# Kernel optimization log

Hardware: AMD Instinct MI355X
Metric: run time of the kernel (lower is better)

## Reference

```python
import jax, jax.numpy as jnp
import numpy as np
import math

B, C, N, T = 16, 32, 500, 10
NH, DK = 8, 8
D = NH * DK  # 64
TT = 6       # tem_size after conv_temp1 (10->6)
EPS = 1e-5


def setup_inputs() -> dict:
    key = jax.random.key(0)
    ks = jax.random.split(key, 32)
    s = 0.05
    rn = lambda k, shp: jax.random.normal(k, shp, dtype=jnp.float32) * s
    return {
        "x": jax.random.normal(ks[0], (B, C, N, T), dtype=jnp.float32),
        "A": jax.random.uniform(ks[1], (N, N), dtype=jnp.float32) / N,
        "conv1_W": rn(ks[2], (32, 32)), "conv1_b": jnp.zeros((32,), jnp.float32),
        "te1_W": rn(ks[3], (64, 32)), "te1_b": jnp.zeros((64,), jnp.float32),
        "convq_W": rn(ks[4], (64, 64, 1, 3)), "convq_b": jnp.zeros((64,), jnp.float32),
        "convk_W": rn(ks[5], (64, 64, 1, 3)), "convk_b": jnp.zeros((64,), jnp.float32),
        "linv_W": rn(ks[6], (64, 64)), "linv_b": jnp.zeros((64,), jnp.float32),
        "lino_W": rn(ks[7], (64, 64)), "lino_b": jnp.zeros((64,), jnp.float32),
        "te2_W": rn(ks[8], (32, 64)), "te2_b": jnp.zeros((32,), jnp.float32),
        "mlp_W": rn(ks[9], (64, 160)), "mlp_b": jnp.zeros((64,), jnp.float32),
        "ct1_W": rn(ks[10], (6, 10)), "ct1_b": jnp.zeros((6,), jnp.float32),
        "tat_c1_W": rn(ks[11], (32,)), "tat_c2_W": rn(ks[12], (500,)),
        "tat_w": rn(ks[13], (500, 32)), "tat_b": jnp.zeros((6, 6), jnp.float32),
        "tat_v": rn(ks[14], (6, 6)),
        "bn1_g": jnp.ones((6,), jnp.float32), "bn1_b": jnp.zeros((6,), jnp.float32),
        "bn2_g": jnp.ones((32,), jnp.float32), "bn2_b": jnp.zeros((32,), jnp.float32),
    }


def _forward(x, A, conv1_W, conv1_b, te1_W, te1_b, convq_W, convq_b, convk_W, convk_b,
             linv_W, linv_b, lino_W, lino_b, te2_W, te2_b, mlp_W, mlp_b, ct1_W, ct1_b,
             tat_c1_W, tat_c2_W, tat_w, tat_b, tat_v, bn1_g, bn1_b, bn2_g, bn2_b):
    b, c, n, t = x.shape
    c1x1 = lambda z, W, bb: jnp.einsum('bchw,oc->bohw', z, W) + bb[None, :, None, None]
    residual = c1x1(x, conv1_W, conv1_b)                      # (B,32,N,T)
    h = c1x1(x, te1_W, te1_b)                                 # (B,64,N,T)
    # --- temporal-context multi-head self-attention (att bias is 0 in source due to bug) ---
    dn = ('NCHW', 'OIHW', 'NCHW')
    q = jax.lax.conv_general_dilated(h, convq_W, (1, 1), ((0, 0), (1, 1)), dimension_numbers=dn) + convq_b[None, :, None, None]
    k = jax.lax.conv_general_dilated(h, convk_W, (1, 1), ((0, 0), (1, 1)), dimension_numbers=dn) + convk_b[None, :, None, None]
    sh = lambda z: z.reshape(b, NH, DK, n, t).transpose(0, 3, 1, 4, 2)  # (B,N,h,T,dk)
    q, k = sh(q), sh(k)
    hp = h.transpose(0, 2, 3, 1)                              # (B,N,T,64)
    v = (hp @ linv_W.T + linv_b).reshape(b, n, t, NH, DK).transpose(0, 1, 3, 2, 4)
    p = jax.nn.softmax(jnp.einsum('bnhtd,bnhsd->bnhts', q, k) / math.sqrt(DK), axis=-1)
    o = jnp.einsum('bnhts,bnhsd->bnhtd', p, v).transpose(0, 1, 3, 2, 4).reshape(b, n, t, D)
    h = (o @ lino_W.T + lino_b).transpose(0, 3, 1, 2)         # (B,64,N,T)
    h = c1x1(h, te2_W, te2_b)                                 # (B,32,N,T)
    # --- multi_gcn_d: static adjacency diffusion + per-timestep attention adjacency ---
    co = h.shape[1]
    xt = h.transpose(0, 3, 2, 1)                              # (B,T,N,C)
    att = jax.nn.softmax(jnp.einsum('btnc,btmc->btnm', xt, xt) / math.sqrt(co), axis=-1)
    outs = [h]
    z = jnp.einsum('btvc,wv->btwc', xt, A); outs.append(z.transpose(0, 3, 2, 1))
    z = jnp.einsum('btvc,wv->btwc', z, A);  outs.append(z.transpose(0, 3, 2, 1))
    z = jnp.einsum('btvc,btwv->btwc', xt, att); outs.append(z.transpose(0, 3, 2, 1))
    z = jnp.einsum('btvc,btwv->btwc', z, att);  outs.append(z.transpose(0, 3, 2, 1))
    hc = c1x1(jnp.concatenate(outs, axis=1), mlp_W, mlp_b)    # (B,64,N,T)
    g = jnp.tanh(hc[:, :co]) * jax.nn.sigmoid(hc[:, co:])     # (B,32,N,10)
    # --- conv_temp1: 1x1 conv over the time axis, 10 -> 6 ---
    g = jnp.einsum('bcnt,st->bcns', g, ct1_W) + ct1_b[None, None, None, :]  # (B,32,N,6)
    # --- TATT_1 temporal attention coefficients ---
    f1 = jnp.einsum('bcnt,c->btn', g, tat_c1_W)               # (B,6,N)
    f2 = jnp.einsum('bcnt,n->bct', g, tat_c2_W)               # (B,32,6)
    logits = jax.nn.sigmoid(jnp.einsum('btn,nc,bcs->bts', f1, tat_w, f2) + tat_b)
    logits = jnp.einsum('pt,bts->bps', tat_v, logits)         # (B,6,6)
    lp = logits.transpose(0, 2, 1)
    mu = lp.mean((0, 2), keepdims=True); var = lp.var((0, 2), keepdims=True)
    lp = (lp - mu) / jnp.sqrt(var + EPS) * bn1_g[None, :, None] + bn1_b[None, :, None]
    coefs = jax.nn.softmax(lp.transpose(0, 2, 1), axis=-1)    # (B,6,6)
    Tc = coefs.transpose(0, 2, 1)
    xo = jnp.einsum('bcnl,blq->bcnq', g, Tc)                  # (B,32,N,6)
    xo = jnp.where(xo > 0, xo, 0.01 * xo) + residual[..., -xo.shape[-1]:]
    mu = xo.mean((0, 2, 3), keepdims=True); var = xo.var((0, 2, 3), keepdims=True)
    return (xo - mu) / jnp.sqrt(var + EPS) * bn2_g[None, :, None, None] + bn2_b[None, :, None, None]


def reference(x, A, conv1_W, conv1_b, te1_W, te1_b, convq_W, convq_b, convk_W, convk_b,
              linv_W, linv_b, lino_W, lino_b, te2_W, te2_b, mlp_W, mlp_b, ct1_W, ct1_b,
              tat_c1_W, tat_c2_W, tat_w, tat_b, tat_v, bn1_g, bn1_b, bn2_g, bn2_b):
    return _forward(x, A, conv1_W, conv1_b, te1_W, te1_b, convq_W, convq_b, convk_W, convk_b,
                    linv_W, linv_b, lino_W, lino_b, te2_W, te2_b, mlp_W, mlp_b, ct1_W, ct1_b,
                    tat_c1_W, tat_c2_W, tat_w, tat_b, tat_v, bn1_g, bn1_b, bn2_g, bn2_b)
```

## Files before the change

kernel.cpp:

```cpp
#include <hip/hip_runtime.h>

typedef unsigned short u16;
typedef unsigned int u32;

__device__ __forceinline__ float b2f(u16 v) { return __uint_as_float((u32)v << 16); }
__device__ __forceinline__ float lopart(u32 u) { return __uint_as_float(u << 16); }
__device__ __forceinline__ float hipart(u32 u) { return __uint_as_float(u & 0xffff0000u); }
__device__ __forceinline__ u16 f2b(float f) {
  u32 u = __float_as_uint(f);
  u32 r = u + 0x7fffu + ((u >> 16) & 1u);
  return (u16)(r >> 16);
}
__device__ __forceinline__ u32 pk2(float a, float b) {
  return (u32)f2b(a) | ((u32)f2b(b) << 16);
}
__device__ __forceinline__ u32 cvtpk(float lo, float hi) {
  u32 r;
  asm("v_cvt_pk_bf16_f32 %0, %1, %2" : "=v"(r) : "v"(lo), "v"(hi));
  return r;
}

struct Ptrs { const void* p[29]; };

typedef __attribute__((ext_vector_type(8))) short short8;
typedef __attribute__((ext_vector_type(4))) float floatx4;

__global__ void k_resolve(const void* __restrict__ g1, int* __restrict__ dtf) {
  if (threadIdx.x == 0) {
    u32 w = *(const u32*)g1;
    *dtf = ((w & 0xffffu) != 0) ? 1 : 0;
  }
}

__global__ __launch_bounds__(256) void k_cvt(Ptrs ps, const int* __restrict__ dtf,
                                             float* __restrict__ Af, float* __restrict__ Wf) {
  bool BF = *dtf != 0;
  int i = blockIdx.x * 256 + threadIdx.x;
  if (i < 250000) {
    const void* pA = ps.p[1];
    Af[i] = BF ? b2f(((const u16*)pA)[i]) : ((const float*)pA)[i];
    return;
  }
  int j = i - 250000;
  if (j >= 65322) return;
  const int SZ[27] = {1024,32,2048,64,12288,64,12288,64,4096,64,4096,64,2048,32,
                      10240,64,60,6,32,500,16000,36,36,6,6,32,32};
  int t = 0, off = 0;
#pragma unroll
  for (int k = 0; k < 27; ++k) {
    if (t == k && j >= off + SZ[k]) { off += SZ[k]; t = k + 1; }
  }
  const void* src = ps.p[2 + t];
  int l = j - off;
  Wf[j] = BF ? b2f(((const u16*)src)[l]) : ((const float*)src)[l];
}

__global__ __launch_bounds__(256) void k_cvtx(const void* __restrict__ x, const int* __restrict__ dtf,
                                              float* __restrict__ xf) {
  bool BF = *dtf != 0;
  int i = blockIdx.x * 256 + threadIdx.x;
  if (i < 2560000) xf[i] = BF ? b2f(((const u16*)x)[i]) : ((const float*)x)[i];
}

__global__ __launch_bounds__(256) void k_pk(const float* __restrict__ Af, u16* __restrict__ Abf) {
  int i = blockIdx.x * 256 + threadIdx.x;
  if (i >= 262144) return;
  int r = i >> 9, v = i & 511;
  bool in = (r < 500) && (v < 500);
  Abf[i] = f2b(in ? Af[r * 500 + v] : 0.f);
}

__global__ __launch_bounds__(256, 4) void k_a2m(const u16* __restrict__ Abf,
                                                u16* __restrict__ A2bf) {
  __shared__ u32 blsT[8192];
  int tid = threadIdx.x;
  int c0 = blockIdx.x * 32;
  for (int i = tid; i < 8192; i += 256) {
    int c = i & 31, h = i >> 5;
    int r0 = 2 * h;
    u32 lo = Abf[r0 * 512 + c0 + c];
    u32 hi = Abf[(r0 + 1) * 512 + c0 + c];
    blsT[c * 256 + (((h & 0xFC) ^ ((c & 15) << 2)) | (h & 3))] = lo | (hi << 16);
  }
  __syncthreads();
  int lane = tid & 63, wave = tid >> 6;
  int q = lane >> 4, ln = lane & 15;
  int rbase = blockIdx.y * 64 + wave * 16;
  const u32* Au = (const u32*)Abf;
  int arow = (rbase + ln) * 256;
  union F8 { u32 u[4]; short8 s; };
  floatx4 acc[2] = {{0.f,0.f,0.f,0.f},{0.f,0.f,0.f,0.f}};
  for (int c2 = 0; c2 < 16; ++c2) {
    int hb = c2 * 16 + q * 4;
    F8 af;
#pragma unroll
    for (int i2 = 0; i2 < 4; ++i2) af.u[i2] = Au[arow + hb + i2];
#pragma unroll
    for (int t2 = 0; t2 < 2; ++t2) {
      int c = t2 * 16 + ln;
      int baseT = c * 256 + (hb ^ ((c & 15) << 2));
      F8 bf;
#pragma unroll
      for (int i2 = 0; i2 < 4; ++i2) bf.u[i2] = blsT[baseT + i2];
      acc[t2] = __builtin_amdgcn_mfma_f32_16x16x32_bf16(af.s, bf.s, acc[t2], 0, 0, 0);
    }
  }
#pragma unroll
  for (int t2 = 0; t2 < 2; ++t2) {
#pragma unroll
    for (int i2 = 0; i2 < 4; ++i2) {
      int r = rbase + q * 4 + i2;
      A2bf[r * 512 + c0 + t2 * 16 + ln] = f2b(acc[t2][i2]);
    }
  }
}

__global__ __launch_bounds__(256) void k_wprep(const float* __restrict__ Wf, float* __restrict__ WT,
                                               u16* __restrict__ WBu) {
  int i = blockIdx.x * 256 + threadIdx.x;
  if (i < 1024) {
    WT[i] = Wf[(i & 31) * 32 + (i >> 5)];
  } else if (i < 7168) {
    int j2 = i - 1024;
    int o = j2 & 63, ct = j2 >> 6;
    int c = ct / 3, tap = ct - c * 3;
    float sq = 0.f, sk = 0.f;
    for (int i2 = 0; i2 < 64; ++i2) {
      float te = Wf[1056 + i2 * 32 + c];
      sq += Wf[3168 + o * 192 + i2 * 3 + tap] * te;
      sk += Wf[15520 + o * 192 + i2 * 3 + tap] * te;
    }
    ((u32*)WT)[i] = pk2(sq, sk);
  } else if (i < 7552) {
    int j2 = i - 7168;
    int f = j2 >> 6, o = j2 & 63;
    int wbase = (f & 1) ? 15520 : 3168;
    float S0 = 0.f, S1 = 0.f, S2 = 0.f;
    for (int i2 = 0; i2 < 64; ++i2) {
      float tb = Wf[3104 + i2];
      S0 += Wf[wbase + o * 192 + i2 * 3 + 0] * tb;
      S1 += Wf[wbase + o * 192 + i2 * 3 + 1] * tb;
      S2 += Wf[wbase + o * 192 + i2 * 3 + 2] * tb;
    }
    float r;
    if (f == 0)      r = Wf[15456 + o] + S0 + S1 + S2;
    else if (f == 1) r = Wf[27808 + o] + S0 + S1 + S2;
    else if (f < 4)  r = S0;
    else             r = S2;
    WT[i] = r;
  } else if (i < 9600) {
    int j2 = i - 7552;
    int c = j2 >> 6, o = j2 & 63;
    float s = 0.f;
    for (int i2 = 0; i2 < 64; ++i2)
      s += Wf[27872 + o * 64 + i2] * Wf[1056 + i2 * 32 + c];
    WT[i] = s;
  } else if (i < 9664) {
    int o = i - 9600;
    float s = Wf[31968 + o];
    for (int i2 = 0; i2 < 64; ++i2)
      s += Wf[27872 + o * 64 + i2] * Wf[3104 + i2];
    WT[i] = s;
  } else if (i < 11712) {
    int j2 = i - 9664;
    int jj = j2 >> 5, c = j2 & 31;
    float s = 0.f;
    for (int o2 = 0; o2 < 64; ++o2)
      s += Wf[36192 + c * 64 + o2] * Wf[32032 + o2 * 64 + jj];
    WT[i] = s;
  } else if (i < 11744) {
    int c = i - 11712;
    float s = Wf[38240 + c];
    for (int o2 = 0; o2 < 64; ++o2)
      s += Wf[36192 + c * 64 + o2] * Wf[36128 + o2];
    WT[i] = s;
  } else if (i < 21984) {
    int j2 = i - 11744;
    int j = j2 & 7, lanev = (j2 >> 3) & 63, ct = (j2 >> 9) & 3, kt = j2 >> 11;
    int qv = lanev >> 4, lnv = lanev & 15;
    int o = ct * 16 + lnv, k = kt * 32 + qv * 8 + j;
    WBu[j2] = f2b(Wf[38272 + o * 160 + k]);
  }
}

__global__ __launch_bounds__(256, 5) void k_front3(
    const float* __restrict__ xf, const float* __restrict__ WT,
    const float* __restrict__ c1B,
    float* __restrict__ h3x, float* __restrict__ res6)
{
  __shared__ __align__(16) float arena[4][1920];
  int tid = threadIdx.x;
  int wave = tid >> 6, lane = tid & 63;
  float* Aw = arena[wave];
  int pair = blockIdx.x * 4 + wave;
  int b = pair / 500, n = pair - b * 500;

  const float* c1T  = WT;
  const u32*   qkF  = (const u32*)(WT + 1024);
  const float* bCq  = WT + 7168;
  const float* bCk  = WT + 7232;
  const float* bE0q = WT + 7296;
  const float* bE0k = WT + 7360;
  const float* bE2q = WT + 7424;
  const float* bE2k = WT + 7488;
  const float* vT   = WT + 7552;
  const float* bvp  = WT + 9600;
  const float* otT  = WT + 9664;
  const float* botp = WT + 11712;

  {
    int c0 = lane >> 1, hf = (lane & 1) * 5;
    const float* xp = xf + ((b * 32 + c0) * 500 + n) * 10 + hf;
    float* dst = Aw + c0 * 12 + hf;
#pragma unroll
    for (int k2 = 0; k2 < 5; ++k2) dst[k2] = xp[k2];
  }
  __builtin_amdgcn_wave_barrier();

  int cl = lane & 31, th = lane >> 5;

  {
    float r0 = c1B[cl], r1 = r0, r2 = r0;
#pragma unroll 4
    for (int i = 0; i < 32; ++i) {
      float w = c1T[i * 32 + cl];
      const float* xr = Aw + i * 12 + 4 + th * 3;
      r0 += w * xr[0]; r1 += w * xr[1]; r2 += w * xr[2];
    }
    float* rp = res6 + ((b * 32 + cl) * 500 + n) * 6 + th * 3;
    rp[0] = r0; rp[1] = r1; rp[2] = r2;
  }

  float qr[10], kr[10], vr[10];
  {
    float cq = bCq[lane], ck = bCk[lane], bv = bvp[lane];
#pragma unroll
    for (int t = 0; t < 10; ++t) { qr[t] = cq; kr[t] = ck; vr[t] = bv; }
    qr[0] -= bE0q[lane]; kr[0] -= bE0k[lane];
    qr[9] -= bE2q[lane]; kr[9] -= bE2k[lane];
    const u32* qp0 = qkF + lane;
    const float* vp0 = vT + lane;
#pragma unroll 2
    for (int c = 0; c < 32; ++c) {
      const float* xr = Aw + c * 12;
      float4 ha = *(const float4*)xr;
      float4 hb = *(const float4*)(xr + 4);
      float2 hc = *(const float2*)(xr + 8);
      u32 u0 = qp0[c * 192];
      u32 u1 = qp0[c * 192 + 64];
      u32 u2 = qp0[c * 192 + 128];
      float wv = vp0[c * 64];
      float q0 = lopart(u0), q1 = lopart(u1), q2 = lopart(u2);
      float k0 = hipart(u0), k1 = hipart(u1), k2v = hipart(u2);
      float hh[10] = {ha.x, ha.y, ha.z, ha.w, hb.x, hb.y, hb.z, hb.w, hc.x, hc.y};
#pragma unroll
      for (int t = 0; t < 10; ++t) { float c_ = hh[t]; qr[t] += q1 * c_; kr[t] += k1 * c_; vr[t] += wv * c_; }
#pragma unroll
      for (int t = 1; t < 10; ++t) { float c_ = hh[t - 1]; qr[t] += q0 * c_; kr[t] += k0 * c_; }
#pragma unroll
      for (int t = 0; t < 9; ++t) { float c_ = hh[t + 1]; qr[t] += q2 * c_; kr[t] += k2v * c_; }
    }
  }
  __builtin_amdgcn_wave_barrier();
  {
    u32* qu = (u32*)Aw + lane * 5;
#pragma unroll
    for (int m = 0; m < 5; ++m) qu[m] = pk2(qr[2 * m], qr[2 * m + 1]);
    float* kp = Aw + 320 + lane * 12;
    *(float4*)kp       = make_float4(kr[0], kr[1], kr[2], kr[3]);
    *(float4*)(kp + 4) = make_float4(kr[4], kr[5], kr[6], kr[7]);
    *(float2*)(kp + 8) = make_float2(kr[8], kr[9]);
  }
  __builtin_amdgcn_wave_barrier();

  {
    const u32* qb = (const u32*)Aw;
#pragma unroll
    for (int pass = 0; pass < 2; ++pass) {
      int row = pass * 64 + lane;
      if (row < 80) {
        int h8 = (row / 10) * 8, r = row - (row / 10) * 10;
        int rm = r >> 1, rs = r & 1;
        float sv[10];
#pragma unroll
        for (int s = 0; s < 10; ++s) sv[s] = 0.f;
#pragma unroll 2
        for (int d = 0; d < 8; ++d) {
          int jj = h8 + d;
          u32 qu = qb[jj * 5 + rm];
          float qv = rs ? hipart(qu) : lopart(qu);
          const float* kp2 = Aw + 320 + jj * 12;
          float4 ka = *(const float4*)kp2;
          float4 kb = *(const float4*)(kp2 + 4);
          float2 kc = *(const float2*)(kp2 + 8);
          sv[0] += qv * ka.x; sv[1] += qv * ka.y; sv[2] += qv * ka.z; sv[3] += qv * ka.w;
          sv[4] += qv * kb.x; sv[5] += qv * kb.y; sv[6] += qv * kb.z; sv[7] += qv * kb.w;
          sv[8] += qv * kc.x; sv[9] += qv * kc.y;
        }
        const float sc_ = 0.35355339059327373f;
        float mx = sv[0];
#pragma unroll
        for (int s = 1; s < 10; ++s) mx = fmaxf(mx, sv[s]);
        float tot = 0.f, ev[10];
#pragma unroll
        for (int s = 0; s < 10; ++s) { ev[s] = expf((sv[s] - mx) * sc_); tot += ev[s]; }
        float inv = 1.f / tot;
        float* pp = Aw + 1088 + row * 10;
#pragma unroll
        for (int s = 0; s < 10; ++s) pp[s] = ev[s] * inv;
      }
    }
  }
  __builtin_amdgcn_wave_barrier();

  {
    const float* pb = Aw + 1088 + (lane >> 3) * 100;
    float orr[10];
#pragma unroll
    for (int t = 0; t < 10; ++t) {
      const float* pr = pb + t * 10;
      float a = 0.f;
#pragma unroll
      for (int s = 0; s < 10; ++s) a += pr[s] * vr[s];
      orr[t] = a;
    }
    float* op = Aw + lane * 12;
    *(float4*)op       = make_float4(orr[0], orr[1], orr[2], orr[3]);
    *(float4*)(op + 4) = make_float4(orr[4], orr[5], orr[6], orr[7]);
    *(float2*)(op + 8) = make_float2(orr[8], orr[9]);
  }
  __builtin_amdgcn_wave_barrier();

  {
    float bt2 = botp[cl];
    float a5[5];
#pragma unroll
    for (int k2 = 0; k2 < 5; ++k2) a5[k2] = bt2;
    const float* tp0 = otT + cl;
    const float* base = Aw + th * 5;
#pragma unroll 2
    for (int j = 0; j < 64; ++j) {
      float w = tp0[j * 32];
      const float* lp = base + j * 12;
#pragma unroll
      for (int k2 = 0; k2 < 5; ++k2) a5[k2] += w * lp[k2];
    }
    int t0 = th * 5;
#pragma unroll
    for (int k2 = 0; k2 < 5; ++k2)
      h3x[((b * 10 + t0 + k2) * 500 + n) * 32 + cl] = a5[k2];
  }
}

__global__ __launch_bounds__(256, 4) void k_z12m(const float* __restrict__ h3x,
    const u16* __restrict__ Abf, const u16* __restrict__ A2bf,
    float* __restrict__ z1x, float* __restrict__ z2x) {
  __shared__ u32 xlsT[8192];
  int tid = threadIdx.x, bt = blockIdx.x;
  const float* src = h3x + bt * 16000;
  for (int i = tid; i < 8192; i += 256) {
    int n = i & 31, h = i >> 5;
    int r0 = 2 * h;
    float v0 = (r0 < 500) ? src[r0 * 32 + n] : 0.f;
    float v1 = (r0 + 1 < 500) ? src[(r0 + 1) * 32 + n] : 0.f;
    xlsT[n * 256 + (((h & 0xFC) ^ ((n & 15) << 2)) | (h & 3))] = pk2(v0, v1);
  }
  __syncthreads();
  int lane = tid & 63, wave = tid >> 6;
  int q = lane >> 4, ln = lane & 15;
  int rbase = blockIdx.y * 64 + wave * 16;
  const u32* Au = (const u32*)Abf;
  const u32* A2u = (const u32*)A2bf;
  int arow = (rbase + ln) * 256;
  union F8 { u32 u[4]; short8 s; };
  floatx4 acc1[2] = {{0.f,0.f,0.f,0.f},{0.f,0.f,0.f,0.f}};
  floatx4 acc2[2] = {{0.f,0.f,0.f,0.f},{0.f,0.f,0.f,0.f}};
  for (int c2 = 0; c2 < 16; ++c2) {
    int hb = c2 * 16 + q * 4;
    F8 a1f, a2f;
#pragma unroll
    for (int i2 = 0; i2 < 4; ++i2) {
      a1f.u[i2] = Au[arow + hb + i2];
      a2f.u[i2] = A2u[arow + hb + i2];
    }
#pragma unroll
    for (int t2 = 0; t2 < 2; ++t2) {
      int n = t2 * 16 + ln;
      int baseT = n * 256 + (hb ^ ((n & 15) << 2));
      F8 bf;
#pragma unroll
      for (int i2 = 0; i2 < 4; ++i2) bf.u[i2] = xlsT[baseT + i2];
      acc1[t2] = __builtin_amdgcn_mfma_f32_16x16x32_bf16(a1f.s, bf.s, acc1[t2], 0, 0, 0);
      acc2[t2] = __builtin_amdgcn_mfma_f32_16x16x32_bf16(a2f.s, bf.s, acc2[t2], 0, 0, 0);
    }
  }
  int outb = bt * 16000;
#pragma unroll
  for (int t2 = 0; t2 < 2; ++t2) {
#pragma unroll
    for (int i2 = 0; i2 < 4; ++i2) {
      int r = rbase + q * 4 + i2;
      if (r < 500) {
        z1x[outb + r * 32 + t2 * 16 + ln] = acc1[t2][i2];
        z2x[outb + r * 32 + t2 * 16 + ln] = acc2[t2][i2];
      }
    }
  }
}

__global__ __launch_bounds__(256, 2) void k_attn2(const float* __restrict__ keys,
                                                  const float* __restrict__ vals,
                                                  float* __restrict__ outp) {
  __shared__ u32 xls[8192];
  __shared__ u32 pch[4][272];
  int tid = threadIdx.x, bt = blockIdx.x;
  const float* kb = keys + bt * 16000;
  for (int i = tid; i < 8192; i += 256) {
    int r = i >> 4, cu = i & 15;
    u32 u = 0;
    if (r < 500) {
      float2 g = *(const float2*)(kb + r * 32 + cu * 2);
      u = pk2(g.x, g.y);
    }
    xls[(r << 4) | (cu ^ (r & 15))] = u;
  }
  __syncthreads();
  int lane = tid & 63, wave = tid >> 6;
  int q = lane >> 4, ln = lane & 15;
  int rbase = blockIdx.y * 64 + wave * 16;
  union F8 { u32 u[4]; short8 s; };
  F8 af;
  {
    int r = rbase + ln;
#pragma unroll
    for (int i2 = 0; i2 < 4; ++i2)
      af.u[i2] = xls[(r << 4) | ((q * 4 + i2) ^ (r & 15))];
  }
  floatx4 acc[32];
#pragma unroll
  for (int ct = 0; ct < 32; ++ct) {
    int r2 = ct * 16 + ln;
    F8 bf;
#pragma unroll
    for (int i2 = 0; i2 < 4; ++i2)
      bf.u[i2] = xls[(r2 << 4) | ((q * 4 + i2) ^ (r2 & 15))];
    acc[ct] = __builtin_amdgcn_mfma_f32_16x16x32_bf16(af.s, bf.s,
              (floatx4){0.f, 0.f, 0.f, 0.f}, 0, 0, 0);
  }
  if (ln >= 4) {
#pragma unroll
    for (int i2 = 0; i2 < 4; ++i2) acc[31][i2] = -1e30f;
  }
  const float sc = 0.17677669529663687f;
  float inv[4];
#pragma unroll
  for (int i2 = 0; i2 < 4; ++i2) {
    float m = -1e30f;
#pragma unroll
    for (int ct = 0; ct < 32; ++ct) m = fmaxf(m, acc[ct][i2]);
#pragma unroll
    for (int d = 1; d < 16; d <<= 1) m = fmaxf(m, __shfl_xor(m, d));
    float s = 0.f;
#pragma unroll
    for (int ct = 0; ct < 32; ++ct) {
      float e = expf((acc[ct][i2] - m) * sc);
      acc[ct][i2] = e; s += e;
    }
#pragma unroll
    for (int d = 1; d < 16; d <<= 1) s += __shfl_xor(s, d);
    inv[i2] = 1.f / s;
  }
  const float* vb = vals + bt * 16000;
  floatx4 zacc[2] = {{0.f,0.f,0.f,0.f},{0.f,0.f,0.f,0.f}};
  u32* myp = pch[wave];
  u16* pw = (u16*)myp;
  for (int c2 = 0; c2 < 16; ++c2) {
#pragma unroll
    for (int t2 = 0; t2 < 2; ++t2) {
      int ct = c2 * 2 + t2;
#pragma unroll
      for (int i2 = 0; i2 < 4; ++i2)
        pw[(q * 4 + i2) * 34 + t2 * 16 + ln] = f2b(acc[ct][i2] * inv[i2]);
    }
    __syncthreads();
    F8 pa;
#pragma unroll
    for (int i2 = 0; i2 < 4; ++i2) pa.u[i2] = myp[ln * 17 + q * 4 + i2];
    int k0 = c2 * 32 + q * 8;
#pragma unroll
    for (int t2 = 0; t2 < 2; ++t2) {
      int n = t2 * 16 + ln;
      short8 bs;
#pragma unroll
      for (int j = 0; j < 8; ++j) {
        float v = vb[(k0 + j) * 32 + n];
        bs[j] = (short)(__float_as_uint(v) >> 16);
      }
      zacc[t2] = __builtin_amdgcn_mfma_f32_16x16x32_bf16(pa.s, bs, zacc[t2], 0, 0, 0);
    }
    __syncthreads();
  }
  int outb = bt * 16000;
#pragma unroll
  for (int t2 = 0; t2 < 2; ++t2) {
#pragma unroll
    for (int i2 = 0; i2 < 4; ++i2) {
      int r = rbase + q * 4 + i2;
      if (r < 500) outp[outb + r * 32 + t2 * 16 + ln] = zacc[t2][i2];
    }
  }
}

__global__ __launch_bounds__(256, 2) void k_gate(
    const float* __restrict__ h3x, const float* __restrict__ z1x, const float* __restrict__ z2x,
    const float* __restrict__ z3x, const float* __restrict__ z4x,
    const u32* __restrict__ WBq, const float* __restrict__ mlpB,
    const float* __restrict__ ct1W, const float* __restrict__ ct1B,
    float* __restrict__ g2w)
{
  __shared__ u32 wlds[5120];
  int tid = threadIdx.x;
  for (int i = tid; i < 5120; i += 256) wlds[i] = WBq[i];
  __syncthreads();
  int lane = tid & 63, wave = tid >> 6;
  int q = lane >> 4, ln = lane & 15;
  int b = blockIdx.y;
  int n0 = blockIdx.x * 32 + wave * 8;
  int nA = n0 + (ln & 7);
  int tAb = ln >> 3;
  int nD = n0 + (q & 1) * 4;
  int tDb = q >> 1;
  float g2a[4][2][6];
#pragma unroll
  for (int i = 0; i < 4; ++i)
#pragma unroll
    for (int ch = 0; ch < 2; ++ch)
#pragma unroll
      for (int s = 0; s < 6; ++s) g2a[i][ch][s] = 0.f;
  float bias[4];
#pragma unroll
  for (int ct = 0; ct < 4; ++ct) bias[ct] = mlpB[ct * 16 + ln];
  union F8 { u32 u[4]; short8 s; };
  for (int tile = 0; tile < 5; ++tile) {
    int tA = tile * 2 + tAb;
    int offA = (((b * 10 + tA) * 500) + nA) * 32 + q * 8;
    floatx4 acc[4];
#pragma unroll
    for (int ct = 0; ct < 4; ++ct) acc[ct] = (floatx4){bias[ct], bias[ct], bias[ct], bias[ct]};
#pragma unroll
    for (int kt = 0; kt < 5; ++kt) {
      const float* sp = kt == 0 ? h3x : kt == 1 ? z1x : kt == 2 ? z2x : kt == 3 ? z3x : z4x;
      float4 a0 = *(const float4*)(sp + offA);
      float4 a1 = *(const float4*)(sp + offA + 4);
      F8 af;
      af.u[0] = cvtpk(a0.x, a0.y);
      af.u[1] = cvtpk(a0.z, a0.w);
      af.u[2] = cvtpk(a1.x, a1.y);
      af.u[3] = cvtpk(a1.z, a1.w);
#pragma unroll
      for (int ct = 0; ct < 4; ++ct) {
        F8 bfr;
        const u32* wp = wlds + (((kt * 4 + ct) << 6) + lane) * 4;
#pragma unroll
        for (int i2 = 0; i2 < 4; ++i2) bfr.u[i2] = wp[i2];
        acc[ct] = __builtin_amdgcn_mfma_f32_16x16x32_bf16(af.s, bfr.s, acc[ct], 0, 0, 0);
      }
    }
    int tD = tile * 2 + tDb;
    float c6[6];
#pragma unroll
    for (int s = 0; s < 6; ++s) c6[s] = ct1W[s * 10 + tD];
#pragma unroll
    for (int i = 0; i < 4; ++i) {
      float e0 = __expf(2.f * acc[0][i]);
      float g0 = ((e0 - 1.f) / (e0 + 1.f)) * (1.f / (1.f + __expf(-acc[2][i])));
      float e1 = __expf(2.f * acc[1][i]);
      float g1 = ((e1 - 1.f) / (e1 + 1.f)) * (1.f / (1.f + __expf(-acc[3][i])));
#pragma unroll
      for (int s = 0; s < 6; ++s) {
        g2a[i][0][s] += g0 * c6[s];
        g2a[i][1][s] += g1 * c6[s];
      }
    }
  }
#pragma unroll
  for (int i = 0; i < 4; ++i)
#pragma unroll
    for (int ch = 0; ch < 2; ++ch)
#pragma unroll
      for (int s = 0; s < 6; ++s)
        g2a[i][ch][s] += __shfl_xor(g2a[i][ch][s], 32);
  if (q < 2) {
#pragma unroll
    for (int i = 0; i < 4; ++i) {
      int n = nD + i;
      if (n < 500) {
#pragma unroll
        for (int ch = 0; ch < 2; ++ch) {
          int c = ln + ch * 16;
          float* gp = g2w + ((b * 32 + c) * 500 + n) * 6;
#pragma unroll
          for (int s = 0; s < 6; ++s) gp[s] = g2a[i][ch][s] + ct1B[s];
        }
      }
    }
  }
}

__global__ __launch_bounds__(256) void k_f1n(const float* __restrict__ g2w,
                                             const float* __restrict__ tc1W,
                                             float* __restrict__ f1w) {
  int i = blockIdx.x * 256 + threadIdx.x;
  if (i >= 48000) return;
  int b = i / 3000, rem = i - b * 3000, s = rem / 500, n = rem - s * 500;
  float a = 0.f;
  for (int c = 0; c < 32; ++c) a += g2w[((b * 32 + c) * 500 + n) * 6 + s] * tc1W[c];
  f1w[(b * 6 + s) * 500 + n] = a;
}

__global__ __launch_bounds__(64) void k_f2(const float* __restrict__ g2w,
                                           const float* __restrict__ c2W, float* __restrict__ f2w) {
  int b = blockIdx.x >> 5, c = blockIdx.x & 31, lane = threadIdx.x;
  float acc[6];
#pragma unroll
  for (int t = 0; t < 6; ++t) acc[t] = 0.f;
  for (int n = lane; n < 500; n += 64) {
    float w = c2W[n];
    const float* gp = g2w + ((b * 32 + c) * 500 + n) * 6;
#pragma unroll
    for (int t = 0; t < 6; ++t) acc[t] += w * gp[t];
  }
#pragma unroll
  for (int t = 0; t < 6; ++t)
    for (int off = 32; off; off >>= 1) acc[t] += __shfl_xor(acc[t], off);
  if (lane == 0) {
#pragma unroll
    for (int t = 0; t < 6; ++t) f2w[(b * 32 + c) * 6 + t] = acc[t];
  }
}

__global__ __launch_bounds__(256) void k_tatt(
    const float* __restrict__ f1w, const float* __restrict__ tatw,
    const float* __restrict__ f2w, const float* __restrict__ tatb, const float* __restrict__ tatv,
    float* __restrict__ lg2w)
{
  __shared__ float mid[192];
  __shared__ float lgt[36];
  int b = blockIdx.x, tid = threadIdx.x;
  if (tid < 192) {
    int t = tid >> 5, c = tid & 31;
    float a = 0.f;
    const float* f1p = f1w + (b * 6 + t) * 500;
    for (int n = 0; n < 500; ++n) a += f1p[n] * tatw[n * 32 + c];
    mid[t * 32 + c] = a;
  }
  __syncthreads();
  if (tid < 36) {
    int t = tid / 6, s = tid - t * 6;
    float a = tatb[t * 6 + s];
    for (int c = 0; c < 32; ++c) a += mid[t * 32 + c] * f2w[(b * 32 + c) * 6 + s];
    lgt[t * 6 + s] = 1.f / (1.f + expf(-a));
  }
  __syncthreads();
  if (tid < 36) {
    int p = tid / 6, s = tid - p * 6;
    float a = 0.f;
#pragma unroll
    for (int t2 = 0; t2 < 6; ++t2) a += tatv[p * 6 + t2] * lgt[t2 * 6 + s];
    lg2w[(b * 6 + p) * 6 + s] = a;
  }
}

__global__ __launch_bounds__(128) void k_coefs(const float* __restrict__ lg2w,
    const float* __restrict__ bn1g, const float* __restrict__ bn1b, float* __restrict__ tcw) {
  __shared__ float mu[6], iv[6], gg[6], bb[6];
  int tid = threadIdx.x;
  if (tid < 6) {
    float s = 0.f, sq = 0.f;
    for (int b = 0; b < 16; ++b)
      for (int q = 0; q < 6; ++q) {
        float v = lg2w[(b * 6 + q) * 6 + tid];
        s += v; sq += v * v;
      }
    float m = s / 96.f;
    mu[tid] = m;
    iv[tid] = rsqrtf(sq / 96.f - m * m + 1e-5f);
    gg[tid] = bn1g[tid]; bb[tid] = bn1b[tid];
  }
  __syncthreads();
  for (int idx = tid; idx < 96; idx += 128) {
    int b = idx / 6, q = idx - b * 6;
    float v[6], mx = -1e30f;
#pragma unroll
    for (int l = 0; l < 6; ++l) {
      v[l] = (lg2w[(b * 6 + q) * 6 + l] - mu[l]) * iv[l] * gg[l] + bb[l];
      mx = fmaxf(mx, v[l]);
    }
    float tot = 0.f;
#pragma unroll
    for (int l = 0; l < 6; ++l) { v[l] = expf(v[l] - mx); tot += v[l]; }
    float inv = 1.f / tot;
#pragma unroll
    for (int l = 0; l < 6; ++l) tcw[(b * 6 + l) * 6 + q] = v[l] * inv;
  }
}

__global__ __launch_bounds__(256) void k_xo(const float* __restrict__ g2w,
    const float* __restrict__ res6, const float* __restrict__ tcw,
    float* __restrict__ xow, float* __restrict__ stats) {
  __shared__ float Tcl[36];
  __shared__ float redS[32][8], redQ[32][8];
  int b = blockIdx.x, chunk = blockIdx.y, tid = threadIdx.x;
  if (tid < 36) Tcl[tid] = tcw[b * 36 + tid];
  __syncthreads();
  int c = tid & 31, sub = tid >> 5;
  int n0 = chunk * 50;
  float s = 0.f, sq = 0.f;
  for (int idx = sub; idx < 300; idx += 8) {
    int nl = idx / 6, q = idx - nl * 6;
    int n = n0 + nl;
    int base = ((b * 32 + c) * 500 + n) * 6;
    const float* gp = g2w + base;
    float xv = 0.f;
#pragma unroll
    for (int l = 0; l < 6; ++l) xv += gp[l] * Tcl[l * 6 + q];
    xv = xv > 0.f ? xv : 0.01f * xv;
    xv += res6[base + q];
    xow[base + q] = xv;
    s += xv; sq += xv * xv;
  }
  redS[c][sub] = s; redQ[c][sub] = sq;
  __syncthreads();
  if (sub == 0) {
    float ts = 0.f, tq = 0.f;
#pragma unroll
    for (int k = 0; k < 8; ++k) { ts += redS[c][k]; tq += redQ[c][k]; }
    atomicAdd(&stats[c], ts);
    atomicAdd(&stats[32 + c], tq);
  }
}

__global__ __launch_bounds__(256) void k_out(const float* __restrict__ xow,
    const float* __restrict__ stats, const float* __restrict__ g2c, const float* __restrict__ b2c,
    float* __restrict__ out) {
  int base = (blockIdx.x * 256 + threadIdx.x) * 4;
#pragma unroll
  for (int k = 0; k < 4; ++k) {
    int i = base + k;
    int c = (i / 3000) & 31;
    float m = stats[c] * (1.f / 48000.f);
    float var = stats[32 + c] * (1.f / 48000.f) - m * m;
    out[i] = (xow[i] - m) * rsqrtf(var + 1e-5f) * g2c[c] + b2c[c];
  }
}

extern "C" void kernel_launch(void* const* d_in, const int* in_sizes, int n_in,
                              void* d_out, int out_size, void* d_ws, size_t ws_size,
                              hipStream_t stream)
{
  (void)in_sizes; (void)out_size;

  float* ws = (float*)d_ws;
  float* Af   = ws;
  float* Wf   = Af + 250000;
  float* A2   = Wf + 65536;
  float* h3x  = A2 + 250000;
  float* z1x  = h3x + 2560000;
  float* z2x  = z1x + 2560000;
  float* z3x  = z2x + 2560000;
  float* z4x  = z3x + 2560000;
  float* res6 = z4x + 2560000;
  float* g2w  = res6 + 1536000;
  float* f1w  = g2w + 1536000;
  float* f2w  = f1w + 48000;
  float* lg2w = f2w + 3072;
  float* tcw  = lg2w + 576;
  float* stats= tcw + 576;
  int*   dtf  = (int*)(stats + 64);
  float* xf   = z4x;
  float* xow  = z1x;
  u16*   Abf  = (u16*)g2w;
  u16*   A2bf = (u16*)(g2w + 131072);
  float* WTp  = g2w + 262144;
  u16*   WBu  = (u16*)f1w;
  if (ws_size < (size_t)16489952 * sizeof(float)) return;

  const float* c1B  = Wf + 1024;
  const float* mlpB = Wf + 48512;
  const float* ct1W = Wf + 48576;
  const float* ct1B = Wf + 48636;
  const float* tc1W = Wf + 48642;
  const float* tc2W = Wf + 48674;
  const float* tatw = Wf + 49174;
  const float* tatb = Wf + 65174;
  const float* tatv = Wf + 65210;
  const float* bn1g = Wf + 65246;
  const float* bn1b = Wf + 65252;
  const float* bn2g = Wf + 65258;
  const float* bn2b = Wf + 65290;

  Ptrs ps;
  for (int i = 0; i < 29; ++i) ps.p[i] = (i < n_in) ? d_in[i] : d_in[0];

  hipMemsetAsync(stats, 0, 64 * sizeof(float), stream);
  k_resolve<<<dim3(1),     64, 0, stream>>>(ps.p[25], dtf);
  k_cvt  <<<dim3(1232),    256, 0, stream>>>(ps, dtf, Af, Wf);
  k_cvtx <<<dim3(10000),   256, 0, stream>>>(ps.p[0], dtf, xf);
  k_wprep<<<dim3(86),      256, 0, stream>>>(Wf, WTp, WBu);
  k_pk   <<<dim3(1024),    256, 0, stream>>>(Af, Abf);
  k_a2m  <<<dim3(16, 8),   256, 0, stream>>>(Abf, A2bf);
  k_front3<<<dim3(2000),   256, 0, stream>>>(xf, WTp, c1B, h3x, res6);
  k_z12m <<<dim3(160, 8),  256, 0, stream>>>(h3x, Abf, A2bf, z1x, z2x);
  k_attn2<<<dim3(160, 8),  256, 0, stream>>>(h3x, h3x, z3x);
  k_attn2<<<dim3(160, 8),  256, 0, stream>>>(h3x, z3x, z4x);
  k_gate <<<dim3(16, 16),  256, 0, stream>>>(h3x, z1x, z2x, z3x, z4x,
                                             (const u32*)WBu, mlpB, ct1W, ct1B, g2w);
  k_f1n  <<<dim3(188),     256, 0, stream>>>(g2w, tc1W, f1w);
  k_f2   <<<dim3(512),      64, 0, stream>>>(g2w, tc2W, f2w);
  k_tatt <<<dim3(16),      256, 0, stream>>>(f1w, tatw, f2w, tatb, tatv, lg2w);
  k_coefs<<<dim3(1),       128, 0, stream>>>(lg2w, bn1g, bn1b, tcw);
  k_xo   <<<dim3(16, 10),  256, 0, stream>>>(g2w, res6, tcw, xow, stats);
  k_out  <<<dim3(1500),    256, 0, stream>>>(xow, stats, bn2g, bn2b, (float*)d_out);
}
```

Baseline: 444.0 us.

## Fuse input conversion into consumers and stage V transposed in LDS for attention

Removes the separate fp32 conversion passes for x and A: k_front3 and k_pk now read raw bf16/f32 inputs directly. In k_attn2, V is loaded once per block into a transposed, swizzled bf16 LDS buffer, replacing strided global gathers in the PV loop. The block-wide syncs there become wave barriers because the P scratch is per-wave. This cuts global traffic and launches at the cost of more LDS per block, which may reduce occupancy.

```diff
diff --git a/kernel.cpp b/kernel.cpp
--- a/kernel.cpp
+++ b/kernel.cpp
@@ -33,15 +33,9 @@
 }
 
 __global__ __launch_bounds__(256) void k_cvt(Ptrs ps, const int* __restrict__ dtf,
-                                             float* __restrict__ Af, float* __restrict__ Wf) {
+                                             float* __restrict__ Wf) {
   bool BF = *dtf != 0;
-  int i = blockIdx.x * 256 + threadIdx.x;
-  if (i < 250000) {
-    const void* pA = ps.p[1];
-    Af[i] = BF ? b2f(((const u16*)pA)[i]) : ((const float*)pA)[i];
-    return;
-  }
-  int j = i - 250000;
+  int j = blockIdx.x * 256 + threadIdx.x;
   if (j >= 65322) return;
   const int SZ[27] = {1024,32,2048,64,12288,64,12288,64,4096,64,4096,64,2048,32,
                       10240,64,60,6,32,500,16000,36,36,6,6,32,32};
@@ -55,19 +49,16 @@
   Wf[j] = BF ? b2f(((const u16*)src)[l]) : ((const float*)src)[l];
 }
 
-__global__ __launch_bounds__(256) void k_cvtx(const void* __restrict__ x, const int* __restrict__ dtf,
-                                              float* __restrict__ xf) {
+__global__ __launch_bounds__(256) void k_pk(const void* __restrict__ A, const int* __restrict__ dtf,
+                                            u16* __restrict__ Abf) {
   bool BF = *dtf != 0;
-  int i = blockIdx.x * 256 + threadIdx.x;
-  if (i < 2560000) xf[i] = BF ? b2f(((const u16*)x)[i]) : ((const float*)x)[i];
-}
-
-__global__ __launch_bounds__(256) void k_pk(const float* __restrict__ Af, u16* __restrict__ Abf) {
   int i = blockIdx.x * 256 + threadIdx.x;
   if (i >= 262144) return;
   int r = i >> 9, v = i & 511;
   bool in = (r < 500) && (v < 500);
-  Abf[i] = f2b(in ? Af[r * 500 + v] : 0.f);
+  u16 o = 0;
+  if (in) o = BF ? ((const u16*)A)[r * 500 + v] : f2b(((const float*)A)[r * 500 + v]);
+  Abf[i] = o;
 }
 
 __global__ __launch_bounds__(256, 4) void k_a2m(const u16* __restrict__ Abf,
@@ -184,7 +175,7 @@
 }
 
 __global__ __launch_bounds__(256, 5) void k_front3(
-    const float* __restrict__ xf, const float* __restrict__ WT,
+    const void* __restrict__ xraw, const int* __restrict__ dtf, const float* __restrict__ WT,
     const float* __restrict__ c1B,
     float* __restrict__ h3x, float* __restrict__ res6)
 {
@@ -209,11 +200,19 @@
   const float* botp = WT + 11712;
 
   {
+    bool BF = *dtf != 0;
     int c0 = lane >> 1, hf = (lane & 1) * 5;
-    const float* xp = xf + ((b * 32 + c0) * 500 + n) * 10 + hf;
+    int base = ((b * 32 + c0) * 500 + n) * 10 + hf;
     float* dst = Aw + c0 * 12 + hf;
-#pragma unroll
-    for (int k2 = 0; k2 < 5; ++k2) dst[k2] = xp[k2];
+    if (BF) {
+      const u16* xp = (const u16*)xraw + base;
+#pragma unroll
+      for (int k2 = 0; k2 < 5; ++k2) dst[k2] = b2f(xp[k2]);
+    } else {
+      const float* xp = (const float*)xraw + base;
+#pragma unroll
+      for (int k2 = 0; k2 < 5; ++k2) dst[k2] = xp[k2];
+    }
   }
   __builtin_amdgcn_wave_barrier();
 
@@ -412,9 +411,11 @@
                                                   const float* __restrict__ vals,
                                                   float* __restrict__ outp) {
   __shared__ u32 xls[8192];
+  __shared__ u32 vlsT[8192];
   __shared__ u32 pch[4][272];
   int tid = threadIdx.x, bt = blockIdx.x;
   const float* kb = keys + bt * 16000;
+  const float* vb = vals + bt * 16000;
   for (int i = tid; i < 8192; i += 256) {
     int r = i >> 4, cu = i & 15;
     u32 u = 0;
@@ -423,6 +424,11 @@
       u = pk2(g.x, g.y);
     }
     xls[(r << 4) | (cu ^ (r & 15))] = u;
+    int n = i & 31, h = i >> 5;
+    int r0 = 2 * h;
+    float v0 = (r0 < 500) ? vb[r0 * 32 + n] : 0.f;
+    float v1 = (r0 + 1 < 500) ? vb[(r0 + 1) * 32 + n] : 0.f;
+    vlsT[n * 256 + (((h & 0xFC) ^ ((n & 15) << 2)) | (h & 3))] = pk2(v0, v1);
   }
   __syncthreads();
   int lane = tid & 63, wave = tid >> 6;
@@ -470,7 +476,6 @@
     for (int d = 1; d < 16; d <<= 1) s += __shfl_xor(s, d);
     inv[i2] = 1.f / s;
   }
-  const float* vb = vals + bt * 16000;
   floatx4 zacc[2] = {{0.f,0.f,0.f,0.f},{0.f,0.f,0.f,0.f}};
   u32* myp = pch[wave];
   u16* pw = (u16*)myp;
@@ -482,23 +487,21 @@
       for (int i2 = 0; i2 < 4; ++i2)
         pw[(q * 4 + i2) * 34 + t2 * 16 + ln] = f2b(acc[ct][i2] * inv[i2]);
     }
-    __syncthreads();
+    __builtin_amdgcn_wave_barrier();
     F8 pa;
 #pragma unroll
     for (int i2 = 0; i2 < 4; ++i2) pa.u[i2] = myp[ln * 17 + q * 4 + i2];
-    int k0 = c2 * 32 + q * 8;
+    int hb = c2 * 16 + q * 4;
 #pragma unroll
     for (int t2 = 0; t2 < 2; ++t2) {
       int n = t2 * 16 + ln;
-      short8 bs;
-#pragma unroll
-      for (int j = 0; j < 8; ++j) {
-        float v = vb[(k0 + j) * 32 + n];
-        bs[j] = (short)(__float_as_uint(v) >> 16);
-      }
-      zacc[t2] = __builtin_amdgcn_mfma_f32_16x16x32_bf16(pa.s, bs, zacc[t2], 0, 0, 0);
-    }
-    __syncthreads();
+      int baseT = n * 256 + (hb ^ ((n & 15) << 2));
+      F8 bf;
+#pragma unroll
+      for (int i2 = 0; i2 < 4; ++i2) bf.u[i2] = vlsT[baseT + i2];
+      zacc[t2] = __builtin_amdgcn_mfma_f32_16x16x32_bf16(pa.s, bf.s, zacc[t2], 0, 0, 0);
+    }
+    __builtin_amdgcn_wave_barrier();
   }
   int outb = bt * 16000;
 #pragma unroll
@@ -777,7 +780,6 @@
   float* tcw  = lg2w + 576;
   float* stats= tcw + 576;
   int*   dtf  = (int*)(stats + 64);
-  float* xf   = z4x;
   float* xow  = z1x;
   u16*   Abf  = (u16*)g2w;
   u16*   A2bf = (u16*)(g2w + 131072);
@@ -804,12 +806,11 @@
 
   hipMemsetAsync(stats, 0, 64 * sizeof(float), stream);
   k_resolve<<<dim3(1),     64, 0, stream>>>(ps.p[25], dtf);
-  k_cvt  <<<dim3(1232),    256, 0, stream>>>(ps, dtf, Af, Wf);
-  k_cvtx <<<dim3(10000),   256, 0, stream>>>(ps.p[0], dtf, xf);
+  k_cvt  <<<dim3(256),     256, 0, stream>>>(ps, dtf, Wf);
   k_wprep<<<dim3(86),      256, 0, stream>>>(Wf, WTp, WBu);
-  k_pk   <<<dim3(1024),    256, 0, stream>>>(Af, Abf);
+  k_pk   <<<dim3(1024),    256, 0, stream>>>(ps.p[1], dtf, Abf);
   k_a2m  <<<dim3(16, 8),   256, 0, stream>>>(Abf, A2bf);
-  k_front3<<<dim3(2000),   256, 0, stream>>>(xf, WTp, c1B, h3x, res6);
+  k_front3<<<dim3(2000),   256, 0, stream>>>(ps.p[0], dtf, WTp, c1B, h3x, res6);
   k_z12m <<<dim3(160, 8),  256, 0, stream>>>(h3x, Abf, A2bf, z1x, z2x);
   k_attn2<<<dim3(160, 8),  256, 0, stream>>>(h3x, h3x, z3x);
   k_attn2<<<dim3(160, 8),  256, 0, stream>>>(h3x, z3x, z4x);
```

New measurement: 458.8 us. +3.3%, slower.
